# Kernel optimization log

Hardware: AMD Instinct MI355X
Metric: run time of the kernel (lower is better)

The kernel has to match this reference:

```python
import jax, jax.numpy as jnp
import numpy as np

N = 50000      # nodes
E = 800000     # edges (avg degree 16)
D_IN = 128
HID = 128
OUT = 64


def setup_inputs() -> dict:
    key = jax.random.key(0)
    ks = jax.random.split(key, 10)
    s = 0.05
    return {
        "node_feats": jax.random.normal(ks[0], (N, D_IN), jnp.float32),
        "edge_index": jax.random.randint(ks[1], (2, E), 0, N, jnp.int32),
        "W1": jax.random.normal(ks[2], (D_IN, HID), jnp.float32) * s,
        "b1": jnp.zeros((HID,), jnp.float32),
        "W2": jax.random.normal(ks[3], (HID, HID), jnp.float32) * s,
        "b2": jnp.zeros((HID,), jnp.float32),
        "W3": jax.random.normal(ks[4], (HID, OUT), jnp.float32) * s,
        "b3": jnp.zeros((OUT,), jnp.float32),
        "skip_W": jax.random.normal(ks[5], (HID, OUT), jnp.float32) * s,
        "skip_b": jnp.zeros((OUT,), jnp.float32),
    }


def _gcn(h, src, dst, out_norm, in_norm, W, b):
    # DGL GraphConv, norm='both': scale src by out_deg^-1/2, sum over incoming
    # edges at dst, scale by in_deg^-1/2, then linear transform + bias.
    h = h * out_norm[:, None]                                   # [N, d]
    agg = jax.ops.segment_sum(h[src], dst, num_segments=N)      # [N, d]
    return (agg * in_norm[:, None]) @ W + b


def reference(node_feats, edge_index, W1, b1, W2, b2, W3, b3, skip_W, skip_b):
    src, dst = edge_index[0], edge_index[1]
    ones = jnp.ones((E,), jnp.float32)
    out_deg = jax.ops.segment_sum(ones, src, num_segments=N)
    in_deg = jax.ops.segment_sum(ones, dst, num_segments=N)
    out_norm = jnp.maximum(out_deg, 1.0) ** -0.5
    in_norm = jnp.maximum(in_deg, 1.0) ** -0.5

    # layer 0 (no skip) + ReLU
    h = jax.nn.relu(_gcn(node_feats, src, dst, out_norm, in_norm, W1, b1))
    # layer 1: same-dim residual blend + ReLU
    g2 = _gcn(h, src, dst, out_norm, in_norm, W2, b2)
    h = jax.nn.relu(0.6 * h + 0.4 * g2)
    # layer 2 (last, no ReLU): dims differ -> projected skip blend
    g3 = _gcn(h, src, dst, out_norm, in_norm, W3, b3)
    h = 0.6 * (h @ skip_W + skip_b) + 0.4 * g3
    return h[None]  # [1, N, OUT]
```

## Files before the change

kernel.cpp:

```cpp
#include <hip/hip_runtime.h>
#include <hip/hip_fp16.h>
#include <math.h>

#define TPB 256
#define CAP 64

typedef _Float16 f16x8 __attribute__((ext_vector_type(8)));
typedef float f32x4 __attribute__((ext_vector_type(4)));

__global__ __launch_bounds__(TPB) void k_count(const int* __restrict__ ei, int E,
                                               int* __restrict__ cnt, int* __restrict__ od,
                                               unsigned short* __restrict__ slots) {
    int t = blockIdx.x * TPB + threadIdx.x;
    int base = t * 4;
    if (base + 3 < E) {
        int4 s4 = *(const int4*)(ei + base);
        int4 d4 = *(const int4*)(ei + E + base);
        int p0 = atomicAdd(&cnt[d4.x], 1);
        int p1 = atomicAdd(&cnt[d4.y], 1);
        int p2 = atomicAdd(&cnt[d4.z], 1);
        int p3 = atomicAdd(&cnt[d4.w], 1);
        atomicAdd(&od[s4.x], 1);
        atomicAdd(&od[s4.y], 1);
        atomicAdd(&od[s4.z], 1);
        atomicAdd(&od[s4.w], 1);
        if (p0 < CAP) slots[(d4.x << 6) + p0] = (unsigned short)s4.x;
        if (p1 < CAP) slots[(d4.y << 6) + p1] = (unsigned short)s4.y;
        if (p2 < CAP) slots[(d4.z << 6) + p2] = (unsigned short)s4.z;
        if (p3 < CAP) slots[(d4.w << 6) + p3] = (unsigned short)s4.w;
    } else {
        for (int e = base; e < E; ++e) {
            int s = ei[e], d = ei[E + e];
            int pos = atomicAdd(&cnt[d], 1);
            if (pos < CAP) slots[(d << 6) + pos] = (unsigned short)s;
            atomicAdd(&od[s], 1);
        }
    }
}

__global__ __launch_bounds__(TPB) void k_norm(const int* __restrict__ od, const int* __restrict__ cnt,
                                              float* __restrict__ onr, float* __restrict__ inr, int N) {
    int i = blockIdx.x * TPB + threadIdx.x;
    if (i < N) {
        onr[i] = 1.0f / sqrtf(fmaxf((float)od[i], 1.0f));
        inr[i] = 1.0f / sqrtf(fmaxf((float)cnt[i], 1.0f));
    }
}

__global__ __launch_bounds__(TPB) void k_cvtw(const float* __restrict__ W1, const float* __restrict__ W2,
                                              const float* __restrict__ Ws, const float* __restrict__ W3,
                                              __half* __restrict__ W1T, __half* __restrict__ W2T,
                                              __half* __restrict__ WCT) {
    int idx = blockIdx.x * TPB + threadIdx.x;
    int m = idx >> 14;
    int r = idx & 16383;
    int j = r >> 7, k = r & 127;
    float v;
    __half* dst;
    if (m == 0)      { v = W1[k * 128 + j]; dst = W1T; }
    else if (m == 1) { v = W2[k * 128 + j]; dst = W2T; }
    else             { v = (j < 64) ? Ws[k * 64 + j] : W3[k * 64 + (j - 64)]; dst = WCT; }
    dst[r] = __float2half(v);
}

__global__ __launch_bounds__(TPB) void k_cvt(const float* __restrict__ x, const float* __restrict__ onr,
                                             __half2* __restrict__ xh, int nF4) {
    int i4 = blockIdx.x * TPB + threadIdx.x;
    if (i4 >= nF4) return;
    int row = i4 >> 5;
    float on = onr[row];
    float4 v = ((const float4*)x)[i4];
    __half2 a = __floats2half2_rn(v.x * on, v.y * on);
    __half2 b = __floats2half2_rn(v.z * on, v.w * on);
    uint2 u;
    u.x = *reinterpret_cast<unsigned int*>(&a);
    u.y = *reinterpret_cast<unsigned int*>(&b);
    ((uint2*)xh)[i4] = u;
}

__global__ __launch_bounds__(TPB) void k_spmmh(const __half2* __restrict__ hp,
                                               const int* __restrict__ cnt,
                                               const unsigned short* __restrict__ slots,
                                               const float* __restrict__ inr,
                                               __half2* __restrict__ aggh, int N) {
    int lane = threadIdx.x & 63;
    int r = blockIdx.x * 4 + (threadIdx.x >> 6);
    if (r >= N) return;
    int n = cnt[r]; if (n > CAP) n = CAP;
    const unsigned short* sl = slots + (r << 6);
    float ax0 = 0.f, ay0 = 0.f, ax1 = 0.f, ay1 = 0.f;
    float ax2 = 0.f, ay2 = 0.f, ax3 = 0.f, ay3 = 0.f;
    int e = 0;
    for (; e + 7 < n; e += 8) {
        ushort4 qa = *(const ushort4*)(sl + e);
        ushort4 qb = *(const ushort4*)(sl + e + 4);
        float2 f0 = __half22float2(hp[qa.x * 64 + lane]);
        float2 f1 = __half22float2(hp[qa.y * 64 + lane]);
        float2 f2 = __half22float2(hp[qa.z * 64 + lane]);
        float2 f3 = __half22float2(hp[qa.w * 64 + lane]);
        float2 f4 = __half22float2(hp[qb.x * 64 + lane]);
        float2 f5 = __half22float2(hp[qb.y * 64 + lane]);
        float2 f6 = __half22float2(hp[qb.z * 64 + lane]);
        float2 f7 = __half22float2(hp[qb.w * 64 + lane]);
        ax0 += f0.x + f1.x;  ay0 += f0.y + f1.y;
        ax1 += f2.x + f3.x;  ay1 += f2.y + f3.y;
        ax2 += f4.x + f5.x;  ay2 += f4.y + f5.y;
        ax3 += f6.x + f7.x;  ay3 += f6.y + f7.y;
    }
    for (; e + 3 < n; e += 4) {
        ushort4 qa = *(const ushort4*)(sl + e);
        float2 f0 = __half22float2(hp[qa.x * 64 + lane]);
        float2 f1 = __half22float2(hp[qa.y * 64 + lane]);
        float2 f2 = __half22float2(hp[qa.z * 64 + lane]);
        float2 f3 = __half22float2(hp[qa.w * 64 + lane]);
        ax0 += f0.x + f1.x;  ay0 += f0.y + f1.y;
        ax1 += f2.x + f3.x;  ay1 += f2.y + f3.y;
    }
    for (; e < n; ++e) {
        float2 f0 = __half22float2(hp[sl[e] * 64 + lane]);
        ax0 += f0.x;  ay0 += f0.y;
    }
    float sc = inr[r];
    aggh[r * 64 + lane] =
        __floats2half2_rn(sc * ((ax0 + ax1) + (ax2 + ax3)), sc * ((ay0 + ay1) + (ay2 + ay3)));
}

__global__ __launch_bounds__(TPB) void k_spmm_final(const float* __restrict__ Pskip,
                                                    const __half* __restrict__ Ph,
                                                    const int* __restrict__ cnt,
                                                    const unsigned short* __restrict__ slots,
                                                    const float* __restrict__ inr,
                                                    const float* __restrict__ b3, const float* __restrict__ bs,
                                                    float* __restrict__ out, int N) {
    int lane = threadIdx.x & 63;
    int r = blockIdx.x * 4 + (threadIdx.x >> 6);
    if (r >= N) return;
    int n = cnt[r]; if (n > CAP) n = CAP;
    const unsigned short* sl = slots + (r << 6);
    float a0 = 0.f, a1 = 0.f, a2 = 0.f, a3 = 0.f;
    float a4 = 0.f, a5 = 0.f, a6 = 0.f, a7 = 0.f;
    int e = 0;
    for (; e + 7 < n; e += 8) {
        ushort4 qa = *(const ushort4*)(sl + e);
        ushort4 qb = *(const ushort4*)(sl + e + 4);
        a0 += __half2float(Ph[qa.x * 64 + lane]);
        a1 += __half2float(Ph[qa.y * 64 + lane]);
        a2 += __half2float(Ph[qa.z * 64 + lane]);
        a3 += __half2float(Ph[qa.w * 64 + lane]);
        a4 += __half2float(Ph[qb.x * 64 + lane]);
        a5 += __half2float(Ph[qb.y * 64 + lane]);
        a6 += __half2float(Ph[qb.z * 64 + lane]);
        a7 += __half2float(Ph[qb.w * 64 + lane]);
    }
    for (; e + 3 < n; e += 4) {
        ushort4 qa = *(const ushort4*)(sl + e);
        a0 += __half2float(Ph[qa.x * 64 + lane]);
        a1 += __half2float(Ph[qa.y * 64 + lane]);
        a2 += __half2float(Ph[qa.z * 64 + lane]);
        a3 += __half2float(Ph[qa.w * 64 + lane]);
    }
    for (; e < n; ++e) a0 += __half2float(Ph[sl[e] * 64 + lane]);
    float g3 = inr[r] * (((a0 + a1) + (a2 + a3)) + ((a4 + a5) + (a6 + a7))) + b3[lane];
    float skip = Pskip[r * 64 + lane] + bs[lane];
    out[r * 64 + lane] = 0.6f * skip + 0.4f * g3;
}

template <int MODE>
__global__ __launch_bounds__(TPB) void k_mgemm(const __half* __restrict__ Ah,
                                               const __half* __restrict__ WT,
                                               const float* __restrict__ bias,
                                               const float* __restrict__ Hres,
                                               const float* __restrict__ onr,
                                               float* __restrict__ Cf, __half* __restrict__ Chh,
                                               int N) {
    __shared__ _Float16 As[64][136];
    int t = threadIdx.x;
    int bm = blockIdx.x * 64;
#pragma unroll
    for (int rep = 0; rep < 4; ++rep) {
        int c = rep * TPB + t;
        int row = c >> 4, cc = c & 15;
        int grow = bm + row;
        f16x8 v = {0, 0, 0, 0, 0, 0, 0, 0};
        if (grow < N) v = *(const f16x8*)(Ah + (size_t)grow * 128 + cc * 8);
        *(f16x8*)(&As[row][cc * 8]) = v;
    }
    __syncthreads();
    int l = t & 63;
    int w = t >> 6;
    int wrow = w * 16;
    int lr = l & 15;
    int lk = (l >> 4) * 8;
    f32x4 acc[8];
    f32x4 zero = {0.f, 0.f, 0.f, 0.f};
#pragma unroll
    for (int j = 0; j < 8; ++j) acc[j] = zero;
#pragma unroll
    for (int kk = 0; kk < 4; ++kk) {
        f16x8 af = *(const f16x8*)(&As[wrow + lr][kk * 32 + lk]);
#pragma unroll
        for (int jt = 0; jt < 8; ++jt) {
            f16x8 bf = *(const f16x8*)(WT + (size_t)(jt * 16 + lr) * 128 + kk * 32 + lk);
            acc[jt] = __builtin_amdgcn_mfma_f32_16x16x32_f16(af, bf, acc[jt], 0, 0, 0);
        }
    }
    int r0 = (l >> 4) * 4;
    float onr4[4];
    if (MODE == 0 || MODE == 2) {
#pragma unroll
        for (int r = 0; r < 4; ++r) {
            int row = bm + wrow + r0 + r;
            onr4[r] = (row < N) ? onr[row] : 0.f;
        }
    }
#pragma unroll
    for (int jt = 0; jt < 8; ++jt) {
        int col = jt * 16 + lr;
        float bv = 0.f;
        if (MODE != 2) bv = bias[col];
#pragma unroll
        for (int r = 0; r < 4; ++r) {
            int row = bm + wrow + r0 + r;
            if (row >= N) continue;
            float v = acc[jt][r] + bv;
            if (MODE == 0) {
                v = fmaxf(v, 0.f);
                Cf[(size_t)row * 128 + col] = v;
                Chh[(size_t)row * 128 + col] = __float2half(v * onr4[r]);
            } else if (MODE == 1) {
                float h1 = Hres[(size_t)row * 128 + col];
                v = fmaxf(0.6f * h1 + 0.4f * v, 0.f);
                Chh[(size_t)row * 128 + col] = __float2half(v);
            } else {
                if (jt < 4) Cf[(size_t)row * 64 + col] = v;
                else        Chh[(size_t)row * 64 + (col - 64)] = __float2half(v * onr4[r]);
            }
        }
    }
}

extern "C" void kernel_launch(void* const* d_in, const int* in_sizes, int n_in,
                              void* d_out, int out_size, void* d_ws, size_t ws_size,
                              hipStream_t stream) {
    const float* x  = (const float*)d_in[0];
    const int*   ei = (const int*)d_in[1];
    const float* W1 = (const float*)d_in[2];
    const float* b1 = (const float*)d_in[3];
    const float* W2 = (const float*)d_in[4];
    const float* b2 = (const float*)d_in[5];
    const float* W3 = (const float*)d_in[6];
    const float* b3 = (const float*)d_in[7];
    const float* Ws = (const float*)d_in[8];
    const float* bs = (const float*)d_in[9];
    float* out = (float*)d_out;

    int N = in_sizes[0] / 128;
    int E = in_sizes[1] / 2;

    char* p = (char*)d_ws;
    auto alloc = [&](size_t bytes) -> char* {
        char* r = p;
        p += (bytes + 255) & ~(size_t)255;
        return r;
    };
    size_t npad = ((size_t)N * 4 + 255) & ~(size_t)255;
    int*   cnt  = (int*)alloc(npad);
    int*   od   = (int*)alloc(npad);
    float* onr  = (float*)alloc((size_t)N * 4);
    float* inr  = (float*)alloc((size_t)N * 4);
    __half* W1T = (__half*)alloc(128 * 128 * 2);
    __half* W2T = (__half*)alloc(128 * 128 * 2);
    __half* WCT = (__half*)alloc(128 * 128 * 2);
    unsigned short* slots = (unsigned short*)alloc((size_t)N * CAP * 2);
    __half* xh   = (__half*)alloc((size_t)N * 128 * 2);
    __half* aggh = (__half*)alloc((size_t)N * 128 * 2);
    float*  h1s  = (float*)alloc((size_t)N * 128 * 4);
    __half* h1h  = (__half*)alloc((size_t)N * 128 * 2);
    (void)ws_size; (void)n_in; (void)out_size;

    float*  Pskip = (float*)xh;
    __half* Ph    = (__half*)aggh;
    __half* h2h   = h1h;

    int cBlocks = ((E + 3) / 4 + TPB - 1) / TPB;
    int nBlocks = (N + TPB - 1) / TPB;
    int cvtBlocks = (N * 32 + TPB - 1) / TPB;
    int spmmBlocks = (N + 3) / 4;
    int mgemmBlocks = (N + 63) / 64;

    hipMemsetAsync(cnt, 0, npad * 2, stream);

    k_count<<<cBlocks, TPB, 0, stream>>>(ei, E, cnt, od, slots);
    k_norm<<<nBlocks, TPB, 0, stream>>>(od, cnt, onr, inr, N);
    k_cvtw<<<192, TPB, 0, stream>>>(W1, W2, Ws, W3, W1T, W2T, WCT);
    k_cvt<<<cvtBlocks, TPB, 0, stream>>>(x, onr, (__half2*)xh, N * 32);

    k_spmmh<<<spmmBlocks, TPB, 0, stream>>>((const __half2*)xh, cnt, slots, inr, (__half2*)aggh, N);
    k_mgemm<0><<<mgemmBlocks, TPB, 0, stream>>>(aggh, W1T, b1, nullptr, onr, h1s, h1h, N);
    k_spmmh<<<spmmBlocks, TPB, 0, stream>>>((const __half2*)h1h, cnt, slots, inr, (__half2*)aggh, N);
    k_mgemm<1><<<mgemmBlocks, TPB, 0, stream>>>(aggh, W2T, b2, h1s, onr, nullptr, h2h, N);
    k_mgemm<2><<<mgemmBlocks, TPB, 0, stream>>>(h2h, WCT, nullptr, nullptr, onr, Pskip, Ph, N);
    k_spmm_final<<<spmmBlocks, TPB, 0, stream>>>(Pskip, Ph, cnt, slots, inr, b3, bs, out, N);
}
```

Measured before the change: 334.5 us.

## Split SpMM gathers into feature-column chunks with edge-parallel lanes

Each SpMM pass now runs as several launches, and each launch handles only one 16-half2 (64-byte) column slice of the feature rows. Inside a wavefront, four groups of 16 lanes each take a different edge and are combined with cross-lane shuffles. The goal is a smaller gathered working set per pass so it fits in L2/cache, plus nontemporal loads of slot indices and nontemporal output stores. In exchange, slot lists are re-read once per chunk, there are more kernel launches, and each gather is only 64 bytes wide with masked-off lanes on ragged edge counts.

```diff
diff --git a/kernel.cpp b/kernel.cpp
--- a/kernel.cpp
+++ b/kernel.cpp
@@ -78,91 +78,73 @@
     ((uint2*)xh)[i4] = u;
 }
 
-__global__ __launch_bounds__(TPB) void k_spmmh(const __half2* __restrict__ hp,
+__global__ __launch_bounds__(TPB) void k_spmmc(const __half2* __restrict__ hp,
                                                const int* __restrict__ cnt,
                                                const unsigned short* __restrict__ slots,
                                                const float* __restrict__ inr,
-                                               __half2* __restrict__ aggh, int N) {
-    int lane = threadIdx.x & 63;
+                                               __half2* __restrict__ aggh, int N, int cb) {
+    int l = threadIdx.x & 63;
     int r = blockIdx.x * 4 + (threadIdx.x >> 6);
     if (r >= N) return;
     int n = cnt[r]; if (n > CAP) n = CAP;
     const unsigned short* sl = slots + (r << 6);
-    float ax0 = 0.f, ay0 = 0.f, ax1 = 0.f, ay1 = 0.f;
-    float ax2 = 0.f, ay2 = 0.f, ax3 = 0.f, ay3 = 0.f;
-    int e = 0;
-    for (; e + 7 < n; e += 8) {
-        ushort4 qa = *(const ushort4*)(sl + e);
-        ushort4 qb = *(const ushort4*)(sl + e + 4);
-        float2 f0 = __half22float2(hp[qa.x * 64 + lane]);
-        float2 f1 = __half22float2(hp[qa.y * 64 + lane]);
-        float2 f2 = __half22float2(hp[qa.z * 64 + lane]);
-        float2 f3 = __half22float2(hp[qa.w * 64 + lane]);
-        float2 f4 = __half22float2(hp[qb.x * 64 + lane]);
-        float2 f5 = __half22float2(hp[qb.y * 64 + lane]);
-        float2 f6 = __half22float2(hp[qb.z * 64 + lane]);
-        float2 f7 = __half22float2(hp[qb.w * 64 + lane]);
-        ax0 += f0.x + f1.x;  ay0 += f0.y + f1.y;
-        ax1 += f2.x + f3.x;  ay1 += f2.y + f3.y;
-        ax2 += f4.x + f5.x;  ay2 += f4.y + f5.y;
-        ax3 += f6.x + f7.x;  ay3 += f6.y + f7.y;
-    }
-    for (; e + 3 < n; e += 4) {
-        ushort4 qa = *(const ushort4*)(sl + e);
-        float2 f0 = __half22float2(hp[qa.x * 64 + lane]);
-        float2 f1 = __half22float2(hp[qa.y * 64 + lane]);
-        float2 f2 = __half22float2(hp[qa.z * 64 + lane]);
-        float2 f3 = __half22float2(hp[qa.w * 64 + lane]);
-        ax0 += f0.x + f1.x;  ay0 += f0.y + f1.y;
-        ax1 += f2.x + f3.x;  ay1 += f2.y + f3.y;
-    }
-    for (; e < n; ++e) {
-        float2 f0 = __half22float2(hp[sl[e] * 64 + lane]);
-        ax0 += f0.x;  ay0 += f0.y;
-    }
-    float sc = inr[r];
-    aggh[r * 64 + lane] =
-        __floats2half2_rn(sc * ((ax0 + ax1) + (ax2 + ax3)), sc * ((ay0 + ay1) + (ay2 + ay3)));
-}
-
-__global__ __launch_bounds__(TPB) void k_spmm_final(const float* __restrict__ Pskip,
-                                                    const __half* __restrict__ Ph,
-                                                    const int* __restrict__ cnt,
-                                                    const unsigned short* __restrict__ slots,
-                                                    const float* __restrict__ inr,
-                                                    const float* __restrict__ b3, const float* __restrict__ bs,
-                                                    float* __restrict__ out, int N) {
-    int lane = threadIdx.x & 63;
+    int g = l >> 4;
+    int f = l & 15;
+    float ax = 0.f, ay = 0.f;
+    for (int e = 0; e < n; e += 4) {
+        int ee = e + g;
+        if (ee < n) {
+            int src = __builtin_nontemporal_load(sl + ee);
+            float2 v = __half22float2(hp[(size_t)src * 64 + cb + f]);
+            ax += v.x;  ay += v.y;
+        }
+    }
+    ax += __shfl_xor(ax, 16, 64);  ay += __shfl_xor(ay, 16, 64);
+    ax += __shfl_xor(ax, 32, 64);  ay += __shfl_xor(ay, 32, 64);
+    if (g == 0) {
+        float sc = inr[r];
+        __half2 o = __floats2half2_rn(sc * ax, sc * ay);
+        unsigned int u = *reinterpret_cast<unsigned int*>(&o);
+        __builtin_nontemporal_store(u, (unsigned int*)(aggh + (size_t)r * 64 + cb + f));
+    }
+}
+
+__global__ __launch_bounds__(TPB) void k_finalc(const float* __restrict__ Pskip,
+                                                const __half2* __restrict__ php,
+                                                const int* __restrict__ cnt,
+                                                const unsigned short* __restrict__ slots,
+                                                const float* __restrict__ inr,
+                                                const float* __restrict__ b3, const float* __restrict__ bs,
+                                                float* __restrict__ out, int N, int ch) {
+    int l = threadIdx.x & 63;
     int r = blockIdx.x * 4 + (threadIdx.x >> 6);
     if (r >= N) return;
     int n = cnt[r]; if (n > CAP) n = CAP;
     const unsigned short* sl = slots + (r << 6);
-    float a0 = 0.f, a1 = 0.f, a2 = 0.f, a3 = 0.f;
-    float a4 = 0.f, a5 = 0.f, a6 = 0.f, a7 = 0.f;
-    int e = 0;
-    for (; e + 7 < n; e += 8) {
-        ushort4 qa = *(const ushort4*)(sl + e);
-        ushort4 qb = *(const ushort4*)(sl + e + 4);
-        a0 += __half2float(Ph[qa.x * 64 + lane]);
-        a1 += __half2float(Ph[qa.y * 64 + lane]);
-        a2 += __half2float(Ph[qa.z * 64 + lane]);
-        a3 += __half2float(Ph[qa.w * 64 + lane]);
-        a4 += __half2float(Ph[qb.x * 64 + lane]);
-        a5 += __half2float(Ph[qb.y * 64 + lane]);
-        a6 += __half2float(Ph[qb.z * 64 + lane]);
-        a7 += __half2float(Ph[qb.w * 64 + lane]);
-    }
-    for (; e + 3 < n; e += 4) {
-        ushort4 qa = *(const ushort4*)(sl + e);
-        a0 += __half2float(Ph[qa.x * 64 + lane]);
-        a1 += __half2float(Ph[qa.y * 64 + lane]);
-        a2 += __half2float(Ph[qa.z * 64 + lane]);
-        a3 += __half2float(Ph[qa.w * 64 + lane]);
-    }
-    for (; e < n; ++e) a0 += __half2float(Ph[sl[e] * 64 + lane]);
-    float g3 = inr[r] * (((a0 + a1) + (a2 + a3)) + ((a4 + a5) + (a6 + a7))) + b3[lane];
-    float skip = Pskip[r * 64 + lane] + bs[lane];
-    out[r * 64 + lane] = 0.6f * skip + 0.4f * g3;
+    int g = l >> 4;
+    int f = l & 15;
+    float ax = 0.f, ay = 0.f;
+    for (int e = 0; e < n; e += 4) {
+        int ee = e + g;
+        if (ee < n) {
+            int src = __builtin_nontemporal_load(sl + ee);
+            float2 v = __half22float2(php[(size_t)src * 32 + ch + f]);
+            ax += v.x;  ay += v.y;
+        }
+    }
+    ax += __shfl_xor(ax, 16, 64);  ay += __shfl_xor(ay, 16, 64);
+    ax += __shfl_xor(ax, 32, 64);  ay += __shfl_xor(ay, 32, 64);
+    if (g == 0) {
+        float sc = inr[r];
+        float2 b3v = ((const float2*)b3)[ch + f];
+        float2 bsv = ((const float2*)bs)[ch + f];
+        float2 sk = ((const float2*)(Pskip + (size_t)r * 64))[ch + f];
+        float2 o;
+        o.x = 0.6f * (sk.x + bsv.x) + 0.4f * (sc * ax + b3v.x);
+        o.y = 0.6f * (sk.y + bsv.y) + 0.4f * (sc * ay + b3v.y);
+        __builtin_nontemporal_store(o.x, out + (size_t)r * 64 + (ch + f) * 2);
+        __builtin_nontemporal_store(o.y, out + (size_t)r * 64 + (ch + f) * 2 + 1);
+    }
 }
 
 template <int MODE>
@@ -295,10 +277,16 @@
     k_cvtw<<<192, TPB, 0, stream>>>(W1, W2, Ws, W3, W1T, W2T, WCT);
     k_cvt<<<cvtBlocks, TPB, 0, stream>>>(x, onr, (__half2*)xh, N * 32);
 
-    k_spmmh<<<spmmBlocks, TPB, 0, stream>>>((const __half2*)xh, cnt, slots, inr, (__half2*)aggh, N);
+    for (int c = 0; c < 4; ++c)
+        k_spmmc<<<spmmBlocks, TPB, 0, stream>>>((const __half2*)xh, cnt, slots, inr,
+                                                (__half2*)aggh, N, c * 16);
     k_mgemm<0><<<mgemmBlocks, TPB, 0, stream>>>(aggh, W1T, b1, nullptr, onr, h1s, h1h, N);
-    k_spmmh<<<spmmBlocks, TPB, 0, stream>>>((const __half2*)h1h, cnt, slots, inr, (__half2*)aggh, N);
+    for (int c = 0; c < 4; ++c)
+        k_spmmc<<<spmmBlocks, TPB, 0, stream>>>((const __half2*)h1h, cnt, slots, inr,
+                                                (__half2*)aggh, N, c * 16);
     k_mgemm<1><<<mgemmBlocks, TPB, 0, stream>>>(aggh, W2T, b2, h1s, onr, nullptr, h2h, N);
     k_mgemm<2><<<mgemmBlocks, TPB, 0, stream>>>(h2h, WCT, nullptr, nullptr, onr, Pskip, Ph, N);
-    k_spmm_final<<<spmmBlocks, TPB, 0, stream>>>(Pskip, Ph, cnt, slots, inr, b3, bs, out, N);
-}
+    for (int c = 0; c < 2; ++c)
+        k_finalc<<<spmmBlocks, TPB, 0, stream>>>(Pskip, (const __half2*)Ph, cnt, slots, inr,
+                                                 b3, bs, out, N, c * 16);
+}
```

After: 596.2 us. +78.3%, slower.

## Quantize gathered node features to int8 with per-row scales for SpMM

Applied to the files above, without the earlier changes.

Replaces fp16 feature buffers used in neighbor gathers with int8 values plus a per-row float scale, produced by new quantization kernels before each SpMM. Aggregation kernels dequantize on the fly, halving bytes per gathered row. The final layer uses half-wave rows for the 64-wide output. This adds extra quantization passes, per-edge scale loads and lower numerical precision.

```diff
diff --git a/kernel.cpp b/kernel.cpp
--- a/kernel.cpp
+++ b/kernel.cpp
@@ -63,106 +63,161 @@
     dst[r] = __float2half(v);
 }
 
-__global__ __launch_bounds__(TPB) void k_cvt(const float* __restrict__ x, const float* __restrict__ onr,
-                                             __half2* __restrict__ xh, int nF4) {
-    int i4 = blockIdx.x * TPB + threadIdx.x;
-    if (i4 >= nF4) return;
-    int row = i4 >> 5;
-    float on = onr[row];
-    float4 v = ((const float4*)x)[i4];
-    __half2 a = __floats2half2_rn(v.x * on, v.y * on);
-    __half2 b = __floats2half2_rn(v.z * on, v.w * on);
-    uint2 u;
-    u.x = *reinterpret_cast<unsigned int*>(&a);
-    u.y = *reinterpret_cast<unsigned int*>(&b);
-    ((uint2*)xh)[i4] = u;
-}
-
-__global__ __launch_bounds__(TPB) void k_spmmh(const __half2* __restrict__ hp,
+__global__ __launch_bounds__(TPB) void k_quant128(const float* __restrict__ src,
+                                                  const float* __restrict__ onr,
+                                                  char2* __restrict__ q, float* __restrict__ sc, int N) {
+    int l = threadIdx.x & 63;
+    int r = blockIdx.x * 4 + (threadIdx.x >> 6);
+    if (r >= N) return;
+    float on = onr[r];
+    float2 v = ((const float2*)(src + (size_t)r * 128))[l];
+    v.x *= on;  v.y *= on;
+    float m = fmaxf(fabsf(v.x), fabsf(v.y));
+#pragma unroll
+    for (int d = 1; d < 64; d <<= 1) m = fmaxf(m, __shfl_xor(m, d, 64));
+    float inv = (m > 1e-20f) ? 127.0f / m : 0.0f;
+    char2 o;
+    o.x = (signed char)(int)rintf(v.x * inv);
+    o.y = (signed char)(int)rintf(v.y * inv);
+    q[(size_t)r * 64 + l] = o;
+    if (l == 0) sc[r] = m * (1.0f / 127.0f);
+}
+
+__global__ __launch_bounds__(TPB) void k_quant64(const __half2* __restrict__ ph,
+                                                 char2* __restrict__ q, float* __restrict__ sc, int N) {
+    int t = threadIdx.x;
+    int l = t & 63;
+    int f = l & 31;
+    int r = blockIdx.x * 8 + (t >> 6) * 2 + (l >> 5);
+    if (r >= N) return;
+    float2 v = __half22float2(ph[(size_t)r * 32 + f]);
+    float m = fmaxf(fabsf(v.x), fabsf(v.y));
+#pragma unroll
+    for (int d = 1; d < 32; d <<= 1) m = fmaxf(m, __shfl_xor(m, d, 64));
+    float inv = (m > 1e-20f) ? 127.0f / m : 0.0f;
+    char2 o;
+    o.x = (signed char)(int)rintf(v.x * inv);
+    o.y = (signed char)(int)rintf(v.y * inv);
+    q[(size_t)r * 32 + f] = o;
+    if (f == 0) sc[r] = m * (1.0f / 127.0f);
+}
+
+__global__ __launch_bounds__(TPB) void k_spmmq(const char2* __restrict__ qt,
+                                               const float* __restrict__ sc,
                                                const int* __restrict__ cnt,
                                                const unsigned short* __restrict__ slots,
                                                const float* __restrict__ inr,
                                                __half2* __restrict__ aggh, int N) {
-    int lane = threadIdx.x & 63;
+    int l = threadIdx.x & 63;
     int r = blockIdx.x * 4 + (threadIdx.x >> 6);
     if (r >= N) return;
     int n = cnt[r]; if (n > CAP) n = CAP;
     const unsigned short* sl = slots + (r << 6);
+    const char2* base = qt + l;
     float ax0 = 0.f, ay0 = 0.f, ax1 = 0.f, ay1 = 0.f;
     float ax2 = 0.f, ay2 = 0.f, ax3 = 0.f, ay3 = 0.f;
     int e = 0;
     for (; e + 7 < n; e += 8) {
         ushort4 qa = *(const ushort4*)(sl + e);
         ushort4 qb = *(const ushort4*)(sl + e + 4);
-        float2 f0 = __half22float2(hp[qa.x * 64 + lane]);
-        float2 f1 = __half22float2(hp[qa.y * 64 + lane]);
-        float2 f2 = __half22float2(hp[qa.z * 64 + lane]);
-        float2 f3 = __half22float2(hp[qa.w * 64 + lane]);
-        float2 f4 = __half22float2(hp[qb.x * 64 + lane]);
-        float2 f5 = __half22float2(hp[qb.y * 64 + lane]);
-        float2 f6 = __half22float2(hp[qb.z * 64 + lane]);
-        float2 f7 = __half22float2(hp[qb.w * 64 + lane]);
-        ax0 += f0.x + f1.x;  ay0 += f0.y + f1.y;
-        ax1 += f2.x + f3.x;  ay1 += f2.y + f3.y;
-        ax2 += f4.x + f5.x;  ay2 += f4.y + f5.y;
-        ax3 += f6.x + f7.x;  ay3 += f6.y + f7.y;
+        char2 v0 = base[(size_t)qa.x * 64];
+        char2 v1 = base[(size_t)qa.y * 64];
+        char2 v2 = base[(size_t)qa.z * 64];
+        char2 v3 = base[(size_t)qa.w * 64];
+        char2 v4 = base[(size_t)qb.x * 64];
+        char2 v5 = base[(size_t)qb.y * 64];
+        char2 v6 = base[(size_t)qb.z * 64];
+        char2 v7 = base[(size_t)qb.w * 64];
+        float s0 = sc[qa.x], s1 = sc[qa.y], s2 = sc[qa.z], s3 = sc[qa.w];
+        float s4 = sc[qb.x], s5 = sc[qb.y], s6 = sc[qb.z], s7 = sc[qb.w];
+        ax0 += s0 * (float)v0.x + s1 * (float)v1.x;  ay0 += s0 * (float)v0.y + s1 * (float)v1.y;
+        ax1 += s2 * (float)v2.x + s3 * (float)v3.x;  ay1 += s2 * (float)v2.y + s3 * (float)v3.y;
+        ax2 += s4 * (float)v4.x + s5 * (float)v5.x;  ay2 += s4 * (float)v4.y + s5 * (float)v5.y;
+        ax3 += s6 * (float)v6.x + s7 * (float)v7.x;  ay3 += s6 * (float)v6.y + s7 * (float)v7.y;
     }
     for (; e + 3 < n; e += 4) {
         ushort4 qa = *(const ushort4*)(sl + e);
-        float2 f0 = __half22float2(hp[qa.x * 64 + lane]);
-        float2 f1 = __half22float2(hp[qa.y * 64 + lane]);
-        float2 f2 = __half22float2(hp[qa.z * 64 + lane]);
-        float2 f3 = __half22float2(hp[qa.w * 64 + lane]);
-        ax0 += f0.x + f1.x;  ay0 += f0.y + f1.y;
-        ax1 += f2.x + f3.x;  ay1 += f2.y + f3.y;
+        char2 v0 = base[(size_t)qa.x * 64];
+        char2 v1 = base[(size_t)qa.y * 64];
+        char2 v2 = base[(size_t)qa.z * 64];
+        char2 v3 = base[(size_t)qa.w * 64];
+        float s0 = sc[qa.x], s1 = sc[qa.y], s2 = sc[qa.z], s3 = sc[qa.w];
+        ax0 += s0 * (float)v0.x + s1 * (float)v1.x;  ay0 += s0 * (float)v0.y + s1 * (float)v1.y;
+        ax1 += s2 * (float)v2.x + s3 * (float)v3.x;  ay1 += s2 * (float)v2.y + s3 * (float)v3.y;
     }
     for (; e < n; ++e) {
-        float2 f0 = __half22float2(hp[sl[e] * 64 + lane]);
-        ax0 += f0.x;  ay0 += f0.y;
-    }
-    float sc = inr[r];
-    aggh[r * 64 + lane] =
-        __floats2half2_rn(sc * ((ax0 + ax1) + (ax2 + ax3)), sc * ((ay0 + ay1) + (ay2 + ay3)));
-}
-
-__global__ __launch_bounds__(TPB) void k_spmm_final(const float* __restrict__ Pskip,
-                                                    const __half* __restrict__ Ph,
-                                                    const int* __restrict__ cnt,
-                                                    const unsigned short* __restrict__ slots,
-                                                    const float* __restrict__ inr,
-                                                    const float* __restrict__ b3, const float* __restrict__ bs,
-                                                    float* __restrict__ out, int N) {
-    int lane = threadIdx.x & 63;
-    int r = blockIdx.x * 4 + (threadIdx.x >> 6);
+        int s = sl[e];
+        char2 v0 = base[(size_t)s * 64];
+        float s0 = sc[s];
+        ax0 += s0 * (float)v0.x;  ay0 += s0 * (float)v0.y;
+    }
+    float scl = inr[r];
+    aggh[(size_t)r * 64 + l] =
+        __floats2half2_rn(scl * ((ax0 + ax1) + (ax2 + ax3)), scl * ((ay0 + ay1) + (ay2 + ay3)));
+}
+
+__global__ __launch_bounds__(TPB) void k_finalq(const float* __restrict__ Pskip,
+                                                const char2* __restrict__ pq,
+                                                const float* __restrict__ psc,
+                                                const int* __restrict__ cnt,
+                                                const unsigned short* __restrict__ slots,
+                                                const float* __restrict__ inr,
+                                                const float* __restrict__ b3, const float* __restrict__ bs,
+                                                float* __restrict__ out, int N) {
+    int t = threadIdx.x;
+    int l = t & 63;
+    int f = l & 31;
+    int r = blockIdx.x * 8 + (t >> 6) * 2 + (l >> 5);
     if (r >= N) return;
     int n = cnt[r]; if (n > CAP) n = CAP;
     const unsigned short* sl = slots + (r << 6);
-    float a0 = 0.f, a1 = 0.f, a2 = 0.f, a3 = 0.f;
-    float a4 = 0.f, a5 = 0.f, a6 = 0.f, a7 = 0.f;
+    const char2* base = pq + f;
+    float ax0 = 0.f, ay0 = 0.f, ax1 = 0.f, ay1 = 0.f;
     int e = 0;
     for (; e + 7 < n; e += 8) {
         ushort4 qa = *(const ushort4*)(sl + e);
         ushort4 qb = *(const ushort4*)(sl + e + 4);
-        a0 += __half2float(Ph[qa.x * 64 + lane]);
-        a1 += __half2float(Ph[qa.y * 64 + lane]);
-        a2 += __half2float(Ph[qa.z * 64 + lane]);
-        a3 += __half2float(Ph[qa.w * 64 + lane]);
-        a4 += __half2float(Ph[qb.x * 64 + lane]);
-        a5 += __half2float(Ph[qb.y * 64 + lane]);
-        a6 += __half2float(Ph[qb.z * 64 + lane]);
-        a7 += __half2float(Ph[qb.w * 64 + lane]);
+        char2 v0 = base[(size_t)qa.x * 32];
+        char2 v1 = base[(size_t)qa.y * 32];
+        char2 v2 = base[(size_t)qa.z * 32];
+        char2 v3 = base[(size_t)qa.w * 32];
+        char2 v4 = base[(size_t)qb.x * 32];
+        char2 v5 = base[(size_t)qb.y * 32];
+        char2 v6 = base[(size_t)qb.z * 32];
+        char2 v7 = base[(size_t)qb.w * 32];
+        float s0 = psc[qa.x], s1 = psc[qa.y], s2 = psc[qa.z], s3 = psc[qa.w];
+        float s4 = psc[qb.x], s5 = psc[qb.y], s6 = psc[qb.z], s7 = psc[qb.w];
+        ax0 += s0 * (float)v0.x + s1 * (float)v1.x;  ay0 += s0 * (float)v0.y + s1 * (float)v1.y;
+        ax1 += s2 * (float)v2.x + s3 * (float)v3.x;  ay1 += s2 * (float)v2.y + s3 * (float)v3.y;
+        ax0 += s4 * (float)v4.x + s5 * (float)v5.x;  ay0 += s4 * (float)v4.y + s5 * (float)v5.y;
+        ax1 += s6 * (float)v6.x + s7 * (float)v7.x;  ay1 += s6 * (float)v6.y + s7 * (float)v7.y;
     }
     for (; e + 3 < n; e += 4) {
         ushort4 qa = *(const ushort4*)(sl + e);
-        a0 += __half2float(Ph[qa.x * 64 + lane]);
-        a1 += __half2float(Ph[qa.y * 64 + lane]);
-        a2 += __half2float(Ph[qa.z * 64 + lane]);
-        a3 += __half2float(Ph[qa.w * 64 + lane]);
-    }
-    for (; e < n; ++e) a0 += __half2float(Ph[sl[e] * 64 + lane]);
-    float g3 = inr[r] * (((a0 + a1) + (a2 + a3)) + ((a4 + a5) + (a6 + a7))) + b3[lane];
-    float skip = Pskip[r * 64 + lane] + bs[lane];
-    out[r * 64 + lane] = 0.6f * skip + 0.4f * g3;
+        char2 v0 = base[(size_t)qa.x * 32];
+        char2 v1 = base[(size_t)qa.y * 32];
+        char2 v2 = base[(size_t)qa.z * 32];
+        char2 v3 = base[(size_t)qa.w * 32];
+        float s0 = psc[qa.x], s1 = psc[qa.y], s2 = psc[qa.z], s3 = psc[qa.w];
+        ax0 += s0 * (float)v0.x + s1 * (float)v1.x;  ay0 += s0 * (float)v0.y + s1 * (float)v1.y;
+        ax1 += s2 * (float)v2.x + s3 * (float)v3.x;  ay1 += s2 * (float)v2.y + s3 * (float)v3.y;
+    }
+    for (; e < n; ++e) {
+        int s = sl[e];
+        char2 v0 = base[(size_t)s * 32];
+        float s0 = psc[s];
+        ax0 += s0 * (float)v0.x;  ay0 += s0 * (float)v0.y;
+    }
+    float scl = inr[r];
+    float2 b3v = ((const float2*)b3)[f];
+    float2 bsv = ((const float2*)bs)[f];
+    float2 sk = ((const float2*)(Pskip + (size_t)r * 64))[f];
+    float gx = scl * (ax0 + ax1) + b3v.x;
+    float gy = scl * (ay0 + ay1) + b3v.y;
+    float2 o;
+    o.x = 0.6f * (sk.x + bsv.x) + 0.4f * gx;
+    o.y = 0.6f * (sk.y + bsv.y) + 0.4f * gy;
+    ((float2*)(out + (size_t)r * 64))[f] = o;
 }
 
 template <int MODE>
@@ -206,7 +261,7 @@
     }
     int r0 = (l >> 4) * 4;
     float onr4[4];
-    if (MODE == 0 || MODE == 2) {
+    if (MODE == 2) {
 #pragma unroll
         for (int r = 0; r < 4; ++r) {
             int row = bm + wrow + r0 + r;
@@ -226,7 +281,6 @@
             if (MODE == 0) {
                 v = fmaxf(v, 0.f);
                 Cf[(size_t)row * 128 + col] = v;
-                Chh[(size_t)row * 128 + col] = __float2half(v * onr4[r]);
             } else if (MODE == 1) {
                 float h1 = Hres[(size_t)row * 128 + col];
                 v = fmaxf(0.6f * h1 + 0.4f * v, 0.f);
@@ -272,20 +326,24 @@
     __half* W2T = (__half*)alloc(128 * 128 * 2);
     __half* WCT = (__half*)alloc(128 * 128 * 2);
     unsigned short* slots = (unsigned short*)alloc((size_t)N * CAP * 2);
-    __half* xh   = (__half*)alloc((size_t)N * 128 * 2);
+    char2* xq   = (char2*)alloc((size_t)N * 64 * 2);
+    float* xsc  = (float*)alloc((size_t)N * 4);
     __half* aggh = (__half*)alloc((size_t)N * 128 * 2);
     float*  h1s  = (float*)alloc((size_t)N * 128 * 4);
-    __half* h1h  = (__half*)alloc((size_t)N * 128 * 2);
+    char2* h1q  = (char2*)alloc((size_t)N * 64 * 2);
+    float* h1sc = (float*)alloc((size_t)N * 4);
+    __half* h2h  = (__half*)alloc((size_t)N * 128 * 2);
     (void)ws_size; (void)n_in; (void)out_size;
 
-    float*  Pskip = (float*)xh;
-    __half* Ph    = (__half*)aggh;
-    __half* h2h   = h1h;
+    float*  Pskip = (float*)aggh;
+    __half* Ph    = (__half*)xq;
+    char2*  pq    = h1q;
+    float*  psc   = h1sc;
 
     int cBlocks = ((E + 3) / 4 + TPB - 1) / TPB;
     int nBlocks = (N + TPB - 1) / TPB;
-    int cvtBlocks = (N * 32 + TPB - 1) / TPB;
     int spmmBlocks = (N + 3) / 4;
+    int half8Blocks = (N + 7) / 8;
     int mgemmBlocks = (N + 63) / 64;
 
     hipMemsetAsync(cnt, 0, npad * 2, stream);
@@ -293,12 +351,14 @@
     k_count<<<cBlocks, TPB, 0, stream>>>(ei, E, cnt, od, slots);
     k_norm<<<nBlocks, TPB, 0, stream>>>(od, cnt, onr, inr, N);
     k_cvtw<<<192, TPB, 0, stream>>>(W1, W2, Ws, W3, W1T, W2T, WCT);
-    k_cvt<<<cvtBlocks, TPB, 0, stream>>>(x, onr, (__half2*)xh, N * 32);
-
-    k_spmmh<<<spmmBlocks, TPB, 0, stream>>>((const __half2*)xh, cnt, slots, inr, (__half2*)aggh, N);
-    k_mgemm<0><<<mgemmBlocks, TPB, 0, stream>>>(aggh, W1T, b1, nullptr, onr, h1s, h1h, N);
-    k_spmmh<<<spmmBlocks, TPB, 0, stream>>>((const __half2*)h1h, cnt, slots, inr, (__half2*)aggh, N);
+
+    k_quant128<<<spmmBlocks, TPB, 0, stream>>>(x, onr, xq, xsc, N);
+    k_spmmq<<<spmmBlocks, TPB, 0, stream>>>(xq, xsc, cnt, slots, inr, (__half2*)aggh, N);
+    k_mgemm<0><<<mgemmBlocks, TPB, 0, stream>>>(aggh, W1T, b1, nullptr, onr, h1s, nullptr, N);
+    k_quant128<<<spmmBlocks, TPB, 0, stream>>>(h1s, onr, h1q, h1sc, N);
+    k_spmmq<<<spmmBlocks, TPB, 0, stream>>>(h1q, h1sc, cnt, slots, inr, (__half2*)aggh, N);
     k_mgemm<1><<<mgemmBlocks, TPB, 0, stream>>>(aggh, W2T, b2, h1s, onr, nullptr, h2h, N);
     k_mgemm<2><<<mgemmBlocks, TPB, 0, stream>>>(h2h, WCT, nullptr, nullptr, onr, Pskip, Ph, N);
-    k_spmm_final<<<spmmBlocks, TPB, 0, stream>>>(Pskip, Ph, cnt, slots, inr, b3, bs, out, N);
-}
+    k_quant64<<<half8Blocks, TPB, 0, stream>>>((const __half2*)Ph, pq, psc, N);
+    k_finalq<<<half8Blocks, TPB, 0, stream>>>(Pskip, pq, psc, cnt, slots, inr, b3, bs, out, N);
+}
```

After: 338.6 us. About the same (+1.2%).

## Compute out-degree via LDS-privatized histogram blocks instead of global atomics

Applied to the files above, without the earlier changes.

Out-degree counting moves out of the per-edge global atomic path and into extra blocks of the same launch. Each extra block histograms one range of source ids over one slice of the edges in shared memory and writes a partial count array. k_norm then sums the 32 partials per node. This halves the global atomics in the build kernel. In exchange, every histogram block rescans its own edge slice once per node range, and extra partial-array traffic is added. The shared histogram also needs 32KB of LDS per block, which may reduce occupancy for the counting blocks.

```diff
diff --git a/kernel.cpp b/kernel.cpp
--- a/kernel.cpp
+++ b/kernel.cpp
@@ -4,13 +4,37 @@
 
 #define TPB 256
 #define CAP 64
+#define KMAX 8192
+#define QSL 32
 
 typedef _Float16 f16x8 __attribute__((ext_vector_type(8)));
 typedef float f32x4 __attribute__((ext_vector_type(4)));
 
-__global__ __launch_bounds__(TPB) void k_count(const int* __restrict__ ei, int E,
-                                               int* __restrict__ cnt, int* __restrict__ od,
-                                               unsigned short* __restrict__ slots) {
+__global__ __launch_bounds__(TPB) void k_build(const int* __restrict__ ei, int E, int cntBlocks,
+                                               int* __restrict__ cnt, unsigned short* __restrict__ slots,
+                                               int* __restrict__ partial, int N) {
+    __shared__ int h[KMAX];
+    if ((int)blockIdx.x >= cntBlocks) {
+        int b = blockIdx.x - cntBlocks;
+        int P = (N + KMAX - 1) / KMAX;
+        int p = b % P, q = b / P;
+        int lo = p * KMAX;
+        int hi = lo + KMAX; if (hi > N) hi = N;
+        int span = hi - lo;
+        for (int i = threadIdx.x; i < KMAX; i += TPB) h[i] = 0;
+        __syncthreads();
+        int EQ = (E + QSL - 1) / QSL;
+        int e0 = q * EQ;
+        int e1 = e0 + EQ; if (e1 > E) e1 = E;
+        for (int e = e0 + threadIdx.x; e < e1; e += TPB) {
+            unsigned int ss = (unsigned int)(ei[e] - lo);
+            if (ss < (unsigned int)span) atomicAdd(&h[ss], 1);
+        }
+        __syncthreads();
+        for (int i = threadIdx.x; i < span; i += TPB)
+            partial[(size_t)q * N + lo + i] = h[i];
+        return;
+    }
     int t = blockIdx.x * TPB + threadIdx.x;
     int base = t * 4;
     if (base + 3 < E) {
@@ -20,10 +44,6 @@
         int p1 = atomicAdd(&cnt[d4.y], 1);
         int p2 = atomicAdd(&cnt[d4.z], 1);
         int p3 = atomicAdd(&cnt[d4.w], 1);
-        atomicAdd(&od[s4.x], 1);
-        atomicAdd(&od[s4.y], 1);
-        atomicAdd(&od[s4.z], 1);
-        atomicAdd(&od[s4.w], 1);
         if (p0 < CAP) slots[(d4.x << 6) + p0] = (unsigned short)s4.x;
         if (p1 < CAP) slots[(d4.y << 6) + p1] = (unsigned short)s4.y;
         if (p2 < CAP) slots[(d4.z << 6) + p2] = (unsigned short)s4.z;
@@ -33,18 +53,19 @@
             int s = ei[e], d = ei[E + e];
             int pos = atomicAdd(&cnt[d], 1);
             if (pos < CAP) slots[(d << 6) + pos] = (unsigned short)s;
-            atomicAdd(&od[s], 1);
-        }
-    }
-}
-
-__global__ __launch_bounds__(TPB) void k_norm(const int* __restrict__ od, const int* __restrict__ cnt,
+        }
+    }
+}
+
+__global__ __launch_bounds__(TPB) void k_norm(const int* __restrict__ partial, const int* __restrict__ cnt,
                                               float* __restrict__ onr, float* __restrict__ inr, int N) {
     int i = blockIdx.x * TPB + threadIdx.x;
-    if (i < N) {
-        onr[i] = 1.0f / sqrtf(fmaxf((float)od[i], 1.0f));
-        inr[i] = 1.0f / sqrtf(fmaxf((float)cnt[i], 1.0f));
-    }
+    if (i >= N) return;
+    int od = 0;
+#pragma unroll 8
+    for (int q = 0; q < QSL; ++q) od += partial[(size_t)q * N + i];
+    onr[i] = 1.0f / sqrtf(fmaxf((float)od, 1.0f));
+    inr[i] = 1.0f / sqrtf(fmaxf((float)cnt[i], 1.0f));
 }
 
 __global__ __launch_bounds__(TPB) void k_cvtw(const float* __restrict__ W1, const float* __restrict__ W2,
@@ -121,7 +142,7 @@
         ax0 += f0.x;  ay0 += f0.y;
     }
     float sc = inr[r];
-    aggh[r * 64 + lane] =
+    aggh[(size_t)r * 64 + lane] =
         __floats2half2_rn(sc * ((ax0 + ax1) + (ax2 + ax3)), sc * ((ay0 + ay1) + (ay2 + ay3)));
 }
 
@@ -161,8 +182,8 @@
     }
     for (; e < n; ++e) a0 += __half2float(Ph[sl[e] * 64 + lane]);
     float g3 = inr[r] * (((a0 + a1) + (a2 + a3)) + ((a4 + a5) + (a6 + a7))) + b3[lane];
-    float skip = Pskip[r * 64 + lane] + bs[lane];
-    out[r * 64 + lane] = 0.6f * skip + 0.4f * g3;
+    float skip = Pskip[(size_t)r * 64 + lane] + bs[lane];
+    out[(size_t)r * 64 + lane] = 0.6f * skip + 0.4f * g3;
 }
 
 template <int MODE>
@@ -265,7 +286,7 @@
     };
     size_t npad = ((size_t)N * 4 + 255) & ~(size_t)255;
     int*   cnt  = (int*)alloc(npad);
-    int*   od   = (int*)alloc(npad);
+    int*   partial = (int*)alloc((size_t)QSL * N * 4);
     float* onr  = (float*)alloc((size_t)N * 4);
     float* inr  = (float*)alloc((size_t)N * 4);
     __half* W1T = (__half*)alloc(128 * 128 * 2);
@@ -282,16 +303,18 @@
     __half* Ph    = (__half*)aggh;
     __half* h2h   = h1h;
 
-    int cBlocks = ((E + 3) / 4 + TPB - 1) / TPB;
+    int cntBlocks = ((E + 3) / 4 + TPB - 1) / TPB;
+    int P = (N + KMAX - 1) / KMAX;
+    int odBlocks = P * QSL;
     int nBlocks = (N + TPB - 1) / TPB;
     int cvtBlocks = (N * 32 + TPB - 1) / TPB;
     int spmmBlocks = (N + 3) / 4;
     int mgemmBlocks = (N + 63) / 64;
 
-    hipMemsetAsync(cnt, 0, npad * 2, stream);
-
-    k_count<<<cBlocks, TPB, 0, stream>>>(ei, E, cnt, od, slots);
-    k_norm<<<nBlocks, TPB, 0, stream>>>(od, cnt, onr, inr, N);
+    hipMemsetAsync(cnt, 0, npad, stream);
+
+    k_build<<<cntBlocks + odBlocks, TPB, 0, stream>>>(ei, E, cntBlocks, cnt, slots, partial, N);
+    k_norm<<<nBlocks, TPB, 0, stream>>>(partial, cnt, onr, inr, N);
     k_cvtw<<<192, TPB, 0, stream>>>(W1, W2, Ws, W3, W1T, W2T, WCT);
     k_cvt<<<cvtBlocks, TPB, 0, stream>>>(x, onr, (__half2*)xh, N * 32);
 
```

Result: no change. 334.7 us (+0.1%).
